# Kernel tuning notes

Hardware: AMD Instinct MI355X
Metric: run time of the kernel (lower is better)

Reference implementation:

```python
import jax, jax.numpy as jnp
import numpy as np

BIG_NUMBER = 1e7   # repo constant used to mask padded adjacency slots
MAX_ITERS = 32     # params['flow_iters']


def _build_graph(B, N, D, valid_deg, seed=0):
    """Random d-regular-ish graph: each valid slot d holds a permutation of nodes,
    so every node has exactly `valid_deg` in-edges. in_indices[b,v,d] = (b,u,s)
    such that adj[b,u,s] == v. Padded slots (d >= valid_deg) hold the sentinel N
    and their in_indices point to a padded (near-zero-weight) flow entry."""
    rng = np.random.default_rng(seed)
    adj = np.full((B, N, D), N, dtype=np.int32)
    in_idx = np.zeros((B, N, D, 3), dtype=np.int32)
    in_idx[..., 0] = np.arange(B, dtype=np.int32)[:, None, None]
    in_idx[..., 2] = valid_deg  # padded slots -> flow[b, 0, valid_deg] (weight ~ 0)
    for b in range(B):
        for d in range(valid_deg):
            perm = rng.permutation(N).astype(np.int32)
            adj[b, :, d] = perm                      # edge u -> perm[u] via slot d
            inv = np.argsort(perm).astype(np.int32)  # inv[v] = u with perm[u] == v
            in_idx[b, :, d, 1] = inv
            in_idx[b, :, d, 2] = d
    return jnp.asarray(adj), jnp.asarray(in_idx)


def setup_inputs():
    B, N, D, VALID = 4, 100000, 16, 12
    key = jax.random.key(0)
    k1, k2 = jax.random.split(key)
    adj_lst, in_indices = _build_graph(B, N, D, VALID)
    return {
        "flow_proportions": jax.random.normal(k1, (B, N, D), dtype=jnp.float32),
        "demands": jax.random.normal(k2, (B, N, 1), dtype=jnp.float32),
        "adj_lst": adj_lst,
        "in_indices": in_indices,
        "num_nodes": N,
    }


def reference(flow_proportions, demands, adj_lst, in_indices, num_nodes):
    # --- masked softmax over neighbor slots (padded slots get -BIG_NUMBER) ---
    mask = (adj_lst == num_nodes).astype(flow_proportions.dtype)   # [B,N,D]
    masked = flow_proportions - BIG_NUMBER * mask
    weights = jax.nn.softmax(masked, axis=-1)                      # normalized_weights

    # --- mcf_solver: iterate flow <- weights * relu(inflow - demand) ---
    bidx = in_indices[..., 0]   # [B,N,D] batch index
    src = in_indices[..., 1]    # [B,N,D] source node of d-th in-edge
    slot = in_indices[..., 2]   # [B,N,D] slot of this node in source's adj list

    def step(flow, _):
        # gather incoming edge flows, sum -> inflow per node [B,N,1]
        inflow = flow[bidx, src, slot].sum(axis=-1, keepdims=True)
        new_flow = weights * jax.nn.relu(inflow - demands)
        return new_flow, None

    flow, _ = jax.lax.scan(step, jnp.zeros_like(weights), None, length=MAX_ITERS)
    # flow_cost (loss) = sum over nodes/slots of cost_fn(flow) = flow**2 here:
    # flow_cost = jnp.sum(flow * flow, axis=(1, 2))
    return flow
```

## Files before the change

kernel.cpp:

```cpp
#include <hip/hip_runtime.h>

#define DEG 16
#define E12 12
#define MAX_ITERS 32
#define BLK 1024
#define LDSF 25600
#define JMAX 96

__device__ __forceinline__ float ld_sc0(const float* p) {
    return __hip_atomic_load((float*)p, __ATOMIC_RELAXED, __HIP_MEMORY_SCOPE_AGENT);
}
__device__ __forceinline__ void st_sc0(float* p, float v) {
    __hip_atomic_store(p, v, __ATOMIC_RELAXED, __HIP_MEMORY_SCOPE_AGENT);
}
__device__ __forceinline__ unsigned ld_u32_sc0(const unsigned* p) {
    return __hip_atomic_load((unsigned*)p, __ATOMIC_RELAXED, __HIP_MEMORY_SCOPE_AGENT);
}
__device__ __forceinline__ void st_u32_sc0(unsigned* p, unsigned v) {
    __hip_atomic_store(p, v, __ATOMIC_RELAXED, __HIP_MEMORY_SCOPE_AGENT);
}

__device__ __forceinline__ int get_xcd() {
    unsigned x;
    asm volatile("s_getreg_b32 %0, hwreg(HW_REG_XCC_ID)" : "=s"(x));
    return (int)(x & 7u);
}

__device__ __forceinline__ void grid_barrier(unsigned* cnt, unsigned* gen,
                                             unsigned target, unsigned nblocks) {
    __syncthreads();
    if (threadIdx.x == 0) {
        __threadfence();
        unsigned arrived = __hip_atomic_fetch_add(cnt, 1u, __ATOMIC_ACQ_REL,
                                                  __HIP_MEMORY_SCOPE_AGENT);
        if (arrived == nblocks - 1u) {
            __hip_atomic_store(cnt, 0u, __ATOMIC_RELAXED, __HIP_MEMORY_SCOPE_AGENT);
            __hip_atomic_fetch_add(gen, 1u, __ATOMIC_RELEASE, __HIP_MEMORY_SCOPE_AGENT);
        } else {
            while (__hip_atomic_load(gen, __ATOMIC_RELAXED,
                                     __HIP_MEMORY_SCOPE_AGENT) < target)
                __builtin_amdgcn_s_sleep(2);
        }
        __threadfence();
    }
    __syncthreads();
}

__device__ __forceinline__ void xcd_barrier(unsigned* cnt, unsigned* gen,
                                            unsigned target, unsigned nblocks) {
    __syncthreads();
    if (threadIdx.x == 0) {
        unsigned arrived = __hip_atomic_fetch_add(cnt, 1u, __ATOMIC_RELEASE,
                                                  __HIP_MEMORY_SCOPE_WORKGROUP);
        if (arrived == nblocks - 1u) {
            __hip_atomic_store(cnt, 0u, __ATOMIC_RELAXED,
                               __HIP_MEMORY_SCOPE_WORKGROUP);
            __hip_atomic_fetch_add(gen, 1u, __ATOMIC_RELEASE,
                                   __HIP_MEMORY_SCOPE_WORKGROUP);
        } else {
            while (ld_u32_sc0(gen) < target)
                __builtin_amdgcn_s_sleep(2);
        }
    }
    __syncthreads();
}

__device__ __forceinline__ void softmax_row(const float* __restrict__ fp,
                                            const int* __restrict__ adj,
                                            float* __restrict__ wout,
                                            size_t base, int N) {
    const float4* f4 = (const float4*)(fp + base);
    const int4*   a4 = (const int4*)(adj + base);
    float v[DEG];
#pragma unroll
    for (int k = 0; k < DEG / 4; ++k) {
        float4 f = f4[k];
        int4   a = a4[k];
        v[4*k+0] = (a.x == N) ? f.x - 1e7f : f.x;
        v[4*k+1] = (a.y == N) ? f.y - 1e7f : f.y;
        v[4*k+2] = (a.z == N) ? f.z - 1e7f : f.z;
        v[4*k+3] = (a.w == N) ? f.w - 1e7f : f.w;
    }
    float m = v[0];
#pragma unroll
    for (int j = 1; j < DEG; ++j) m = fmaxf(m, v[j]);
    float s = 0.f;
#pragma unroll
    for (int j = 0; j < DEG; ++j) { v[j] = __expf(v[j] - m); s += v[j]; }
    float inv = 1.f / s;
    float4* w4 = (float4*)(wout + base);
#pragma unroll
    for (int k = 0; k < DEG / 4; ++k) {
        float4 o;
        o.x = v[4*k+0] * inv;
        o.y = v[4*k+1] * inv;
        o.z = v[4*k+2] * inv;
        o.w = v[4*k+3] * inv;
        w4[k] = o;
    }
}

__device__ __forceinline__ float node_acc12(const int* __restrict__ es,
                                            const float* __restrict__ ew,
                                            const float* __restrict__ Rc) {
    const int4*   s4 = (const int4*)es;
    const float4* w4 = (const float4*)ew;
    int4 a = s4[0], b = s4[1], c = s4[2];
    float4 x = w4[0], y = w4[1], z = w4[2];
    float acc;
    acc  = x.x * Rc[a.x];  acc += x.y * Rc[a.y];
    acc += x.z * Rc[a.z];  acc += x.w * Rc[a.w];
    acc += y.x * Rc[b.x];  acc += y.y * Rc[b.y];
    acc += y.z * Rc[b.z];  acc += y.w * Rc[b.w];
    acc += z.x * Rc[c.x];  acc += z.y * Rc[c.y];
    acc += z.z * Rc[c.z];  acc += z.w * Rc[c.w];
    return acc;
}

__device__ __forceinline__ void scale_row(float* __restrict__ wout, int g, float r) {
    float4* w4 = (float4*)(wout + (size_t)g * DEG);
#pragma unroll
    for (int k = 0; k < DEG / 4; ++k) {
        float4 v = w4[k];
        v.x *= r; v.y *= r; v.z *= r; v.w *= r;
        w4[k] = v;
    }
}

__global__ __launch_bounds__(BLK, 4)
void fused7_k(const float* __restrict__ fp, const int* __restrict__ adj,
              const int* __restrict__ in_idx, const float* __restrict__ dem,
              const int* __restrict__ nn, float* __restrict__ wout,
              char* __restrict__ wsb, int nodes) {
    __shared__ float lds[LDSF];
    __shared__ int s_xcd, s_rank, s_mode, s_part, s_jbad;
    __shared__ int s_cm[4];
    __shared__ int s_off[5];

    unsigned* g_cnt  = (unsigned*)(wsb);
    unsigned* g_gen  = (unsigned*)(wsb + 128);
    unsigned* blkcnt = (unsigned*)(wsb + 2304);
    unsigned* ovf    = (unsigned*)(wsb + 2432);
    unsigned* jovf   = (unsigned*)(wsb + 2436);
    int*   e_src   = (int*)(wsb + 4096);
    float* e_w     = (float*)(wsb + 4096 + (size_t)nodes * E12 * 4);
    float* Rf0     = (float*)((char*)e_w + (size_t)nodes * E12 * 4);
    float* Rf1     = Rf0 + nodes;
    float* slices  = Rf1 + nodes;
    uint2* regions = (uint2*)((char*)(slices) + (size_t)nodes * 16);

    const int N   = *nn;
    const int tid = (int)threadIdx.x;
    const int T   = (int)gridDim.x * BLK;
    const unsigned nblocks = gridDim.x;
    unsigned gb = 0;

    if (tid == 0) {
        int x = get_xcd();
        s_xcd  = x;
        s_rank = (int)__hip_atomic_fetch_add(&blkcnt[x], 1u, __ATOMIC_RELAXED,
                                             __HIP_MEMORY_SCOPE_AGENT);
    }
    __syncthreads();
    const int my_xcd  = s_xcd;
    const int my_rank = s_rank;

#pragma unroll
    for (int rep = 0; rep < 2; ++rep) {
        int g = (int)blockIdx.x * BLK + tid + rep * T;
        if (g < nodes) softmax_row(fp, adj, wout, (size_t)g * DEG, N);
    }
    grid_barrier(g_cnt, g_gen, ++gb, nblocks);

#pragma unroll
    for (int rep = 0; rep < 2; ++rep) {
        int g = (int)blockIdx.x * BLK + tid + rep * T;
        if (g >= nodes) continue;
        const int gbat = g / N;
        const int4* t4 = (const int4*)(in_idx + (size_t)g * 48);
        int cb[16], cs[16], cl[16];
#pragma unroll
        for (int q = 0; q < 4; ++q) {
            int4 qa = t4[3*q + 0];
            int4 qb = t4[3*q + 1];
            int4 qc = t4[3*q + 2];
            cb[4*q+0] = qa.x; cs[4*q+0] = qa.y; cl[4*q+0] = qa.z;
            cb[4*q+1] = qa.w; cs[4*q+1] = qb.x; cl[4*q+1] = qb.y;
            cb[4*q+2] = qb.z; cs[4*q+2] = qb.w; cl[4*q+2] = qc.x;
            cb[4*q+3] = qc.y; cs[4*q+3] = qc.z; cl[4*q+3] = qc.w;
        }
        float cw[16];
#pragma unroll
        for (int k = 0; k < 16; ++k)
            cw[k] = wout[((size_t)cb[k] * N + cs[k]) * DEG + cl[k]];
        bool bad = (cw[12] != 0.f) || (cw[13] != 0.f) ||
                   (cw[14] != 0.f) || (cw[15] != 0.f);
#pragma unroll
        for (int k = 0; k < E12; ++k)
            bad = bad || (cb[k] != gbat) || ((unsigned)cs[k] >= (unsigned)N);
        if (bad) st_u32_sc0(ovf, 1u);
        int4*   es4 = (int4*)(e_src + (size_t)g * E12);
        float4* ew4 = (float4*)(e_w + (size_t)g * E12);
        es4[0] = make_int4(cs[0], cs[1], cs[2], cs[3]);
        es4[1] = make_int4(cs[4], cs[5], cs[6], cs[7]);
        es4[2] = make_int4(cs[8], cs[9], cs[10], cs[11]);
        ew4[0] = make_float4(cw[0], cw[1], cw[2], cw[3]);
        ew4[1] = make_float4(cw[4], cw[5], cw[6], cw[7]);
        ew4[2] = make_float4(cw[8], cw[9], cw[10], cw[11]);
    }
    grid_barrier(g_cnt, g_gen, ++gb, nblocks);

    const int npb   = (N + 31) >> 5;
    const int nch   = (N + LDSF - 1) / LDSF;
    const int chunk = (N + nch - 1) / nch;
    if (tid == 0) {
        unsigned cc[8];
#pragma unroll
        for (int x = 0; x < 8; ++x) cc[x] = ld_u32_sc0(&blkcnt[x]);
        bool ok = (4 * N == nodes) && (N > 0) && (npb <= 4 * BLK) &&
                  (nch >= 1) && (nch <= 4) && (chunk <= LDSF) &&
                  (ld_u32_sc0(ovf) == 0u);
#pragma unroll
        for (int p = 0; p < 4; ++p)
            ok = ok && (cc[2*p] >= 32u || cc[2*p+1] >= 32u);
        s_mode = ok ? 1 : 0;
        s_part = (ok && cc[my_xcd] >= 32u && my_rank < 32) ? 1 : 0;
    }
    __syncthreads();
    const bool fast = (s_mode == 1);
    const bool part = (s_part == 1);

    if (fast) {
        const int batch = my_xcd >> 1;
        const int lbase = my_rank * npb;
        const int lim   = min(lbase + npb, N);
        float d[4];
        int   lno[4];
        bool  act[4];
        float r[4];
        uint2* reg = regions + (size_t)(my_xcd * 32 + my_rank) * (JMAX * BLK);

        if (part) {
            if (tid < 4) s_cm[tid] = 0;
            __syncthreads();
            const int b1 = chunk, b2 = 2 * chunk, b3 = 3 * chunk;
            int c0 = 0, c1 = 0, c2 = 0, c3 = 0;
#pragma unroll
            for (int s = 0; s < 4; ++s) {
                int l = lbase + s * BLK + tid;
                lno[s] = l;
                act[s] = (l < lim);
                d[s] = 0.f;
                if (act[s]) {
                    int g = batch * N + l;
                    d[s] = dem[g];
                    const int* es = e_src + (size_t)g * E12;
#pragma unroll
                    for (int k = 0; k < E12; ++k) {
                        int src = es[k];
                        int c = (src >= b1) + (src >= b2) + (src >= b3);
                        c0 += (c == 0); c1 += (c == 1);
                        c2 += (c == 2); c3 += (c == 3);
                    }
                }
            }
            atomicMax(&s_cm[0], c0); atomicMax(&s_cm[1], c1);
            atomicMax(&s_cm[2], c2); atomicMax(&s_cm[3], c3);
            __syncthreads();
            if (tid == 0) {
                s_off[0] = 0;
                s_off[1] = s_cm[0];
                s_off[2] = s_cm[0] + s_cm[1];
                s_off[3] = s_cm[0] + s_cm[1] + s_cm[2];
                s_off[4] = s_cm[0] + s_cm[1] + s_cm[2] + s_cm[3];
                if (s_off[4] > JMAX) st_u32_sc0(jovf, 1u);
            }
            __syncthreads();
            if (s_off[4] <= JMAX) {
                int cur0 = s_off[0], cur1 = s_off[1],
                    cur2 = s_off[2], cur3 = s_off[3];
#pragma unroll
                for (int s = 0; s < 4; ++s) {
                    if (!act[s]) continue;
                    int g = batch * N + lno[s];
                    const int*   es = e_src + (size_t)g * E12;
                    const float* ew = e_w + (size_t)g * E12;
#pragma unroll
                    for (int k = 0; k < E12; ++k) {
                        int src = es[k];
                        float w = ew[k];
                        int c = (src >= b1) + (src >= b2) + (src >= b3);
                        int j = (c == 0) ? cur0 : (c == 1) ? cur1
                               : (c == 2) ? cur2 : cur3;
                        reg[(size_t)j * BLK + tid] =
                            make_uint2((unsigned)src | ((unsigned)s << 20),
                                       __float_as_uint(w));
                        cur0 += (c == 0); cur1 += (c == 1);
                        cur2 += (c == 2); cur3 += (c == 3);
                    }
                }
                {
                    int cc_[4] = {cur0, cur1, cur2, cur3};
#pragma unroll
                    for (int c = 0; c < 4; ++c) {
                        unsigned ps = (unsigned)(c * chunk);
                        for (int j = cc_[c]; j < s_off[c + 1]; ++j)
                            reg[(size_t)j * BLK + tid] = make_uint2(ps, 0u);
                    }
                }
            }
        }
        grid_barrier(g_cnt, g_gen, ++gb, nblocks);
        if (tid == 0) s_jbad = (int)ld_u32_sc0(jovf);
        __syncthreads();

        if (s_jbad == 0) {
            if (!part) return;
            unsigned* xc = (unsigned*)(wsb + 256 + my_xcd * 256);
            unsigned* xg = (unsigned*)(wsb + 256 + my_xcd * 256 + 128);
            unsigned xb = 0;
            float* bufA = slices + (size_t)(2 * my_xcd + 0) * N;
            float* bufB = slices + (size_t)(2 * my_xcd + 1) * N;

#pragma unroll
            for (int s = 0; s < 4; ++s) {
                r[s] = fmaxf(-d[s], 0.f);
                if (act[s]) st_sc0(bufA + lno[s], r[s]);
            }
            xcd_barrier(xc, xg, ++xb, 32u);

            float* Rin  = bufA;
            float* Rout = bufB;
            for (int t = 1; t < MAX_ITERS; ++t) {
                float a0 = 0.f, a1 = 0.f, a2 = 0.f, a3 = 0.f;
                for (int c = 0; c < nch; ++c) {
                    const int cbase = c * chunk;
                    const int ce = min(chunk, N - cbase);
                    for (int i = tid; i < ce; i += BLK)
                        lds[i] = ld_sc0(Rin + cbase + i);
                    __syncthreads();
                    const int jb = s_off[c], je = s_off[c + 1];
                    for (int j = jb; j < je; ++j) {
                        uint2 pr = reg[(size_t)j * BLK + tid];
                        float w = __uint_as_float(pr.y);
                        int idx = (int)(pr.x & 0xFFFFFu) - cbase;
                        int tg  = (int)(pr.x >> 20);
                        float wv = w * lds[idx];
                        a0 += (tg == 0) ? wv : 0.f;
                        a1 += (tg == 1) ? wv : 0.f;
                        a2 += (tg == 2) ? wv : 0.f;
                        a3 += (tg == 3) ? wv : 0.f;
                    }
                    __syncthreads();
                }
                r[0] = fmaxf(a0 - d[0], 0.f);
                r[1] = fmaxf(a1 - d[1], 0.f);
                r[2] = fmaxf(a2 - d[2], 0.f);
                r[3] = fmaxf(a3 - d[3], 0.f);
                if (t < MAX_ITERS - 1) {
#pragma unroll
                    for (int s = 0; s < 4; ++s)
                        if (act[s]) st_sc0(Rout + lno[s], r[s]);
                    xcd_barrier(xc, xg, ++xb, 32u);
                    float* tmp = Rin; Rin = Rout; Rout = tmp;
                }
            }
#pragma unroll
            for (int s = 0; s < 4; ++s)
                if (act[s]) scale_row(wout, batch * N + lno[s], r[s]);
            return;
        }
    }

    {
        int g0 = (int)blockIdx.x * BLK + tid;
        int g1 = g0 + T;
        bool a0 = (g0 < nodes), a1 = (g1 < nodes);
        float d0 = a0 ? dem[g0] : 0.f;
        float d1 = a1 ? dem[g1] : 0.f;
        int base0 = a0 ? (g0 / N) * N : 0;
        int base1 = a1 ? (g1 / N) * N : 0;
        float r0 = fmaxf(-d0, 0.f), r1 = fmaxf(-d1, 0.f);
        if (a0) Rf0[g0] = r0;
        if (a1) Rf0[g1] = r1;
        grid_barrier(g_cnt, g_gen, ++gb, nblocks);
        const float* Rc = Rf0;
        float*       Rn = Rf1;
        for (int t = 1; t < MAX_ITERS; ++t) {
            if (a0) r0 = fmaxf(node_acc12(e_src + (size_t)g0 * E12,
                                          e_w + (size_t)g0 * E12,
                                          Rc + base0) - d0, 0.f);
            if (a1) r1 = fmaxf(node_acc12(e_src + (size_t)g1 * E12,
                                          e_w + (size_t)g1 * E12,
                                          Rc + base1) - d1, 0.f);
            if (t < MAX_ITERS - 1) {
                if (a0) Rn[g0] = r0;
                if (a1) Rn[g1] = r1;
                grid_barrier(g_cnt, g_gen, ++gb, nblocks);
                float* tmp = (float*)Rc; Rc = Rn; Rn = tmp;
            }
        }
        if (a0) scale_row(wout, g0, r0);
        if (a1) scale_row(wout, g1, r1);
    }
}

__global__ void softmax_k(const float* __restrict__ fp, const int* __restrict__ adj,
                          const int* __restrict__ nn, float* __restrict__ wout,
                          int nodes) {
    int i = blockIdx.x * blockDim.x + threadIdx.x;
    if (i >= nodes) return;
    softmax_row(fp, adj, wout, (size_t)i * DEG, *nn);
}

__global__ void gather_k(const int* __restrict__ in_idx, const float* __restrict__ w,
                         const int* __restrict__ nn, int* __restrict__ e_srcO,
                         float* __restrict__ e_wO, int edges) {
    int e = blockIdx.x * blockDim.x + threadIdx.x;
    if (e >= edges) return;
    const int N = *nn;
    size_t e3 = 3 * (size_t)e;
    int fi = in_idx[e3] * N + in_idx[e3 + 1];
    e_srcO[e] = fi;
    e_wO[e]   = w[(size_t)fi * DEG + in_idx[e3 + 2]];
}

__global__ void iter_k(const int* __restrict__ e_srcO, const float* __restrict__ e_wO,
                       const float* __restrict__ dem, const float* __restrict__ Rin,
                       float* __restrict__ Rout, int nodes) {
    int i = blockIdx.x * blockDim.x + threadIdx.x;
    if (i >= nodes) return;
    const size_t base = (size_t)i * DEG;
    const int4*   s4 = (const int4*)(e_srcO + base);
    const float4* w4 = (const float4*)(e_wO + base);
    float acc = 0.f;
#pragma unroll
    for (int k = 0; k < DEG / 4; ++k) {
        int4   s = s4[k];
        float4 w = w4[k];
        acc += w.x * Rin[s.x];
        acc += w.y * Rin[s.y];
        acc += w.z * Rin[s.z];
        acc += w.w * Rin[s.w];
    }
    float r = acc - dem[i];
    Rout[i] = r > 0.f ? r : 0.f;
}

__global__ void final_k(const float* __restrict__ w, const float* __restrict__ R,
                        float* __restrict__ out, int nodes) {
    int i = blockIdx.x * blockDim.x + threadIdx.x;
    if (i >= nodes) return;
    scale_row((float*)w, i, R[i]);
    (void)out;
}

extern "C" void kernel_launch(void* const* d_in, const int* in_sizes, int n_in,
                              void* d_out, int out_size, void* d_ws, size_t ws_size,
                              hipStream_t stream) {
    const float* fp  = (const float*)d_in[0];
    const float* dem = (const float*)d_in[1];
    const int*   adj = (const int*)d_in[2];
    const int*   idx = (const int*)d_in[3];
    const int*   nn  = (const int*)d_in[4];

    const int edges = in_sizes[0];
    const int nodes = in_sizes[1];

    float* weights = (float*)d_out;
    char*  ws      = (char*)d_ws;

    int dev = 0, cus = 0, maxBlk = 0;
    hipGetDevice(&dev);
    hipDeviceGetAttribute(&cus, hipDeviceAttributeMultiprocessorCount, dev);
    hipOccupancyMaxActiveBlocksPerMultiprocessor(&maxBlk, (const void*)fused7_k,
                                                 BLK, 0);

    const size_t need = 4096 + (size_t)nodes * (E12 * 8 + 8 + 16)
                      + (size_t)256 * JMAX * BLK * 8;
    const int grid = cus;

    const bool fused_ok = (maxBlk >= 1) && (cus >= 16) &&
                          ((long long)grid * BLK * 2 >= nodes) &&
                          (ws_size >= need) && (nodes % 4 == 0);

    if (fused_ok) {
        hipMemsetAsync(ws, 0, 4096, stream);
        void* args[] = { (void*)&fp, (void*)&adj, (void*)&idx, (void*)&dem,
                         (void*)&nn, (void*)&weights, (void*)&ws, (void*)&nodes };
        hipLaunchCooperativeKernel((const void*)fused7_k, dim3(grid), dim3(BLK),
                                   args, 0, stream);
    } else {
        int*   e_srcO = (int*)ws;
        float* e_wO   = (float*)(ws + (size_t)edges * sizeof(int));
        float* R0     = (float*)(ws + (size_t)edges * 8);
        float* R1     = R0 + nodes;
        const int blk = 256;
        const int gn = (nodes + blk - 1) / blk;
        const int ge = (edges + blk - 1) / blk;
        hipMemsetAsync(R0, 0, (size_t)nodes * sizeof(float), stream);
        softmax_k<<<gn, blk, 0, stream>>>(fp, adj, nn, weights, nodes);
        gather_k<<<ge, blk, 0, stream>>>(idx, weights, nn, e_srcO, e_wO, edges);
        float* a = R0;
        float* b = R1;
        for (int t = 0; t < MAX_ITERS; ++t) {
            iter_k<<<gn, blk, 0, stream>>>(e_srcO, e_wO, dem, a, b, nodes);
            float* tmp = a; a = b; b = tmp;
        }
        final_k<<<gn, blk, 0, stream>>>(weights, a, (float*)d_out, nodes);
    }
}
```

Baseline: 1.024 ms.

## Vectorize L2-coherent LDS staging loads and trim per-thread padded region loops

The per-chunk copy of the residual vector into LDS now uses 16-byte global loads carrying the sc0 cache bit, issued two at a time, instead of scalar relaxed atomic loads. Each thread records its own per-chunk entry counts packed into one register, so the gather loop stops at that count and the padding writes to the region buffer during setup are dropped. Residual stores become plain stores. The inline asm places s_waitcnt vmcnt(0) right after every load, which serializes the paired loads. Cross-block visibility now relies on the sc0 load bit and on the barrier's fence rather than on atomic stores. The packed 8-bit counts assume at most 255 entries per chunk.

Measured after the change: 1.027 ms. About the same (+0.3%).

```diff
diff --git a/kernel.cpp b/kernel.cpp
--- a/kernel.cpp
+++ b/kernel.cpp
@@ -7,6 +7,8 @@
 #define LDSF 25600
 #define JMAX 96
 
+typedef float f32x4 __attribute__((ext_vector_type(4)));
+
 __device__ __forceinline__ float ld_sc0(const float* p) {
     return __hip_atomic_load((float*)p, __ATOMIC_RELAXED, __HIP_MEMORY_SCOPE_AGENT);
 }
@@ -18,6 +20,19 @@
 }
 __device__ __forceinline__ void st_u32_sc0(unsigned* p, unsigned v) {
     __hip_atomic_store(p, v, __ATOMIC_RELAXED, __HIP_MEMORY_SCOPE_AGENT);
+}
+
+__device__ __forceinline__ float ld1_l2(const float* p) {
+    float v;
+    asm volatile("global_load_dword %0, %1, off sc0\n\ts_waitcnt vmcnt(0)"
+                 : "=v"(v) : "v"(p) : "memory");
+    return v;
+}
+__device__ __forceinline__ f32x4 ld4_l2(const f32x4* p) {
+    f32x4 v;
+    asm volatile("global_load_dwordx4 %0, %1, off sc0\n\ts_waitcnt vmcnt(0)"
+                 : "=v"(v) : "v"(p) : "memory");
+    return v;
 }
 
 __device__ __forceinline__ int get_xcd() {
@@ -128,11 +143,11 @@
 }
 
 __global__ __launch_bounds__(BLK, 4)
-void fused7_k(const float* __restrict__ fp, const int* __restrict__ adj,
+void fused8_k(const float* __restrict__ fp, const int* __restrict__ adj,
               const int* __restrict__ in_idx, const float* __restrict__ dem,
               const int* __restrict__ nn, float* __restrict__ wout,
               char* __restrict__ wsb, int nodes) {
-    __shared__ float lds[LDSF];
+    __shared__ __align__(16) float lds[LDSF];
     __shared__ int s_xcd, s_rank, s_mode, s_part, s_jbad;
     __shared__ int s_cm[4];
     __shared__ int s_off[5];
@@ -238,6 +253,7 @@
         int   lno[4];
         bool  act[4];
         float r[4];
+        unsigned mycnt = 0;
         uint2* reg = regions + (size_t)(my_xcd * 32 + my_rank) * (JMAX * BLK);
 
         if (part) {
@@ -299,15 +315,10 @@
                         cur2 += (c == 2); cur3 += (c == 3);
                     }
                 }
-                {
-                    int cc_[4] = {cur0, cur1, cur2, cur3};
-#pragma unroll
-                    for (int c = 0; c < 4; ++c) {
-                        unsigned ps = (unsigned)(c * chunk);
-                        for (int j = cc_[c]; j < s_off[c + 1]; ++j)
-                            reg[(size_t)j * BLK + tid] = make_uint2(ps, 0u);
-                    }
-                }
+                mycnt = (unsigned)(cur0 - s_off[0])
+                      | ((unsigned)(cur1 - s_off[1]) << 8)
+                      | ((unsigned)(cur2 - s_off[2]) << 16)
+                      | ((unsigned)(cur3 - s_off[3]) << 24);
             }
         }
         grid_barrier(g_cnt, g_gen, ++gb, nblocks);
@@ -325,7 +336,7 @@
 #pragma unroll
             for (int s = 0; s < 4; ++s) {
                 r[s] = fmaxf(-d[s], 0.f);
-                if (act[s]) st_sc0(bufA + lno[s], r[s]);
+                if (act[s]) bufA[lno[s]] = r[s];
             }
             xcd_barrier(xc, xg, ++xb, 32u);
 
@@ -336,10 +347,29 @@
                 for (int c = 0; c < nch; ++c) {
                     const int cbase = c * chunk;
                     const int ce = min(chunk, N - cbase);
-                    for (int i = tid; i < ce; i += BLK)
-                        lds[i] = ld_sc0(Rin + cbase + i);
+                    const float* src = Rin + cbase;
+                    if ((((size_t)src) & 15) == 0) {
+                        const int n4 = ce >> 2;
+                        f32x4* lds4 = (f32x4*)lds;
+                        const f32x4* s4 = (const f32x4*)src;
+                        int i4 = tid;
+                        for (; i4 + BLK < n4; i4 += 2 * BLK) {
+                            f32x4 va = ld4_l2(s4 + i4);
+                            f32x4 vb = ld4_l2(s4 + i4 + BLK);
+                            lds4[i4] = va;
+                            lds4[i4 + BLK] = vb;
+                        }
+                        for (; i4 < n4; i4 += BLK)
+                            lds4[i4] = ld4_l2(s4 + i4);
+                        for (int i = (n4 << 2) + tid; i < ce; i += BLK)
+                            lds[i] = ld1_l2(src + i);
+                    } else {
+                        for (int i = tid; i < ce; i += BLK)
+                            lds[i] = ld1_l2(src + i);
+                    }
                     __syncthreads();
-                    const int jb = s_off[c], je = s_off[c + 1];
+                    const int jb = s_off[c];
+                    const int je = jb + (int)((mycnt >> (8 * c)) & 255u);
                     for (int j = jb; j < je; ++j) {
                         uint2 pr = reg[(size_t)j * BLK + tid];
                         float w = __uint_as_float(pr.y);
@@ -360,7 +390,7 @@
                 if (t < MAX_ITERS - 1) {
 #pragma unroll
                     for (int s = 0; s < 4; ++s)
-                        if (act[s]) st_sc0(Rout + lno[s], r[s]);
+                        if (act[s]) Rout[lno[s]] = r[s];
                     xcd_barrier(xc, xg, ++xb, 32u);
                     float* tmp = Rin; Rin = Rout; Rout = tmp;
                 }
@@ -473,7 +503,7 @@
     int dev = 0, cus = 0, maxBlk = 0;
     hipGetDevice(&dev);
     hipDeviceGetAttribute(&cus, hipDeviceAttributeMultiprocessorCount, dev);
-    hipOccupancyMaxActiveBlocksPerMultiprocessor(&maxBlk, (const void*)fused7_k,
+    hipOccupancyMaxActiveBlocksPerMultiprocessor(&maxBlk, (const void*)fused8_k,
                                                  BLK, 0);
 
     const size_t need = 4096 + (size_t)nodes * (E12 * 8 + 8 + 16)
@@ -488,7 +518,7 @@
         hipMemsetAsync(ws, 0, 4096, stream);
         void* args[] = { (void*)&fp, (void*)&adj, (void*)&idx, (void*)&dem,
                          (void*)&nn, (void*)&weights, (void*)&ws, (void*)&nodes };
-        hipLaunchCooperativeKernel((const void*)fused7_k, dim3(grid), dim3(BLK),
+        hipLaunchCooperativeKernel((const void*)fused8_k, dim3(grid), dim3(BLK),
                                    args, 0, stream);
     } else {
         int*   e_srcO = (int*)ws;
```
